# Kernel tuning notes

Hardware: AMD Instinct MI355X
Metric: run time of the kernel (lower is better)

The kernel has to match this reference:

```python
import jax, jax.numpy as jnp
import numpy as np

B = 4096
NUM_IMAGES = 10
D = 512
MARGIN = 1.0
EPS = 1e-6  # torch F.pairwise_distance adds eps to the difference elementwise


def _make_triplets():
    # per TripletLoss.generate_subsamples
    i = np.arange(B)
    j = np.arange(1, NUM_IMAGES)
    anchor = np.repeat(i, NUM_IMAGES - 1)                      # [T]
    positive = np.repeat(i * NUM_IMAGES, NUM_IMAGES - 1)       # [T]
    negative = (i[:, None] * NUM_IMAGES + j[None, :]).reshape(-1)  # [T]
    return anchor.astype(np.int64), positive.astype(np.int64), negative.astype(np.int64)


def setup_inputs() -> dict:
    key = jax.random.key(0)
    k1, k2 = jax.random.split(key)
    a, p, n = _make_triplets()
    return {
        "text_embeddings": jax.random.normal(k1, (B, D), dtype=jnp.float32),
        "image_embeddings": jax.random.normal(k2, (B * NUM_IMAGES, D), dtype=jnp.float32),
        "anchor_idx": jnp.asarray(a),
        "positive_idx": jnp.asarray(p),
        "negative_idx": jnpp if False else jnp.asarray(n),
    }


def _pairwise_dist(x, y):
    # torch pairwise_distance: ||x - y + eps||_2
    d = x - y + EPS
    return jnp.sqrt(jnp.sum(d * d, axis=-1))


def reference(text_embeddings, image_embeddings, anchor_idx, positive_idx, negative_idx):
    a = text_embeddings[anchor_idx]       # [T, D]
    p = image_embeddings[positive_idx]    # [T, D]
    n = image_embeddings[negative_idx]    # [T, D]
    d_ap = _pairwise_dist(a, p)           # [T]
    d_an = _pairwise_dist(a, n)           # [T]
    per_triplet = jnp.maximum(d_ap - d_an + MARGIN, 0.0)
    return jnp.mean(per_triplet)
```

## Files before the change

kernel.cpp:

```cpp
#include <hip/hip_runtime.h>


#define BATCH 4096
#define NIMG 10
#define DIM 512
#define NTRIP (BATCH * (NIMG - 1))

static constexpr float kMargin = 1.0f;
static constexpr float kEps = 1e-6f;

__global__ __launch_bounds__(256) void triplet_partial_kernel(
    const float* __restrict__ text,
    const float* __restrict__ img,
    float* __restrict__ partial)
{
    const int gtid = blockIdx.x * blockDim.x + threadIdx.x;
    const int wave = gtid >> 6;
    const int lane = threadIdx.x & 63;

    const float* arow = text + (size_t)wave * DIM + lane * 8;
    const float4 a0 = *(const float4*)(arow);
    const float4 a1 = *(const float4*)(arow + 4);

    const float* ibase = img + (size_t)wave * NIMG * DIM + lane * 8;

    float ssq[NIMG];
#pragma unroll
    for (int j = 0; j < NIMG; ++j) {
        const float* r = ibase + j * DIM;
        const float4 r0 = *(const float4*)(r);
        const float4 r1 = *(const float4*)(r + 4);
        float d0 = a0.x - r0.x + kEps;
        float d1 = a0.y - r0.y + kEps;
        float d2 = a0.z - r0.z + kEps;
        float d3 = a0.w - r0.w + kEps;
        float d4 = a1.x - r1.x + kEps;
        float d5 = a1.y - r1.y + kEps;
        float d6 = a1.z - r1.z + kEps;
        float d7 = a1.w - r1.w + kEps;
        float s = d0 * d0;
        s = fmaf(d1, d1, s);
        s = fmaf(d2, d2, s);
        s = fmaf(d3, d3, s);
        s = fmaf(d4, d4, s);
        s = fmaf(d5, d5, s);
        s = fmaf(d6, d6, s);
        s = fmaf(d7, d7, s);
        ssq[j] = s;
    }

#pragma unroll
    for (int j = 0; j < NIMG; ++j) {
        float v = ssq[j];
#pragma unroll
        for (int off = 32; off > 0; off >>= 1)
            v += __shfl_xor(v, off, 64);
        ssq[j] = v;
    }

    const float d_ap = sqrtf(ssq[0]);
    float loss = 0.0f;
#pragma unroll
    for (int j = 1; j < NIMG; ++j) {
        const float d_an = sqrtf(ssq[j]);
        loss += fmaxf(d_ap - d_an + kMargin, 0.0f);
    }

    if (lane == 0) partial[wave] = loss;
}

__global__ __launch_bounds__(1024) void triplet_reduce_kernel(
    const float* __restrict__ partial, float* __restrict__ out)
{
    __shared__ float wsum[16];
    const float4 v = *(const float4*)(partial + threadIdx.x * 4);
    float s = (v.x + v.y) + (v.z + v.w);
#pragma unroll
    for (int off = 32; off > 0; off >>= 1)
        s += __shfl_xor(s, off, 64);
    const int wid = threadIdx.x >> 6;
    const int lane = threadIdx.x & 63;
    if (lane == 0) wsum[wid] = s;
    __syncthreads();
    if (threadIdx.x < 16) {
        float t = wsum[threadIdx.x];
#pragma unroll
        for (int off = 8; off > 0; off >>= 1)
            t += __shfl_xor(t, off, 64);
        if (threadIdx.x == 0) out[0] = t * (1.0f / (float)NTRIP);
    }
}

extern "C" void kernel_launch(void* const* d_in, const int* in_sizes, int n_in,
                              void* d_out, int out_size, void* d_ws, size_t ws_size,
                              hipStream_t stream) {
    const float* text = (const float*)d_in[0];
    const float* img  = (const float*)d_in[1];
    float* out = (float*)d_out;
    float* partial = (float*)d_ws;

    const int threads = 256;
    const int blocks = BATCH / 4;
    triplet_partial_kernel<<<blocks, threads, 0, stream>>>(text, img, partial);
    triplet_reduce_kernel<<<1, 1024, 0, stream>>>(partial, out);
}
```

Measured before the change: 22.38 us.

## Fuse partial and final reduction into one cooperative kernel with grid sync

```diff
diff --git a/kernel.cpp b/kernel.cpp
--- a/kernel.cpp
+++ b/kernel.cpp
@@ -1,28 +1,30 @@
 #include <hip/hip_runtime.h>
+#include <hip/hip_cooperative_groups.h>
+
+namespace cg = cooperative_groups;
 
 
 #define BATCH 4096
 #define NIMG 10
 #define DIM 512
 #define NTRIP (BATCH * (NIMG - 1))
+#define NBLK 256
+#define THREADS 256
+#define WAVES_PER_BLK (THREADS / 64)
+#define ANCH_PER_WAVE (BATCH / (NBLK * WAVES_PER_BLK))
 
 static constexpr float kMargin = 1.0f;
 static constexpr float kEps = 1e-6f;
 
-__global__ __launch_bounds__(256) void triplet_partial_kernel(
-    const float* __restrict__ text,
-    const float* __restrict__ img,
-    float* __restrict__ partial)
+__device__ __forceinline__ float anchor_loss(
+    const float* __restrict__ text, const float* __restrict__ img,
+    int anchor, int lane)
 {
-    const int gtid = blockIdx.x * blockDim.x + threadIdx.x;
-    const int wave = gtid >> 6;
-    const int lane = threadIdx.x & 63;
-
-    const float* arow = text + (size_t)wave * DIM + lane * 8;
+    const float* arow = text + (size_t)anchor * DIM + lane * 8;
     const float4 a0 = *(const float4*)(arow);
     const float4 a1 = *(const float4*)(arow + 4);
 
-    const float* ibase = img + (size_t)wave * NIMG * DIM + lane * 8;
+    const float* ibase = img + (size_t)anchor * NIMG * DIM + lane * 8;
 
     float ssq[NIMG];
 #pragma unroll
@@ -65,7 +67,59 @@
         const float d_an = sqrtf(ssq[j]);
         loss += fmaxf(d_ap - d_an + kMargin, 0.0f);
     }
+    return loss;
+}
 
+__global__ __launch_bounds__(THREADS) void triplet_coop_kernel(
+    const float* __restrict__ text,
+    const float* __restrict__ img,
+    float* __restrict__ partial,
+    float* __restrict__ out)
+{
+    __shared__ float lsum[WAVES_PER_BLK];
+    __shared__ float wsum[WAVES_PER_BLK];
+
+    const int lane = threadIdx.x & 63;
+    const int wid  = threadIdx.x >> 6;
+    const int gwave = blockIdx.x * WAVES_PER_BLK + wid;
+
+    float wloss = 0.0f;
+#pragma unroll
+    for (int k = 0; k < ANCH_PER_WAVE; ++k)
+        wloss += anchor_loss(text, img, gwave * ANCH_PER_WAVE + k, lane);
+
+    if (lane == 0) lsum[wid] = wloss;
+    __syncthreads();
+    if (threadIdx.x == 0) {
+        const float bs = lsum[0] + lsum[1] + lsum[2] + lsum[3];
+        __hip_atomic_store(&partial[blockIdx.x], bs,
+                           __ATOMIC_RELAXED, __HIP_MEMORY_SCOPE_AGENT);
+    }
+
+    cg::this_grid().sync();
+
+    if (blockIdx.x == 0) {
+        float s = __hip_atomic_load(&partial[threadIdx.x],
+                                    __ATOMIC_RELAXED, __HIP_MEMORY_SCOPE_AGENT);
+#pragma unroll
+        for (int off = 32; off > 0; off >>= 1)
+            s += __shfl_xor(s, off, 64);
+        if (lane == 0) wsum[wid] = s;
+        __syncthreads();
+        if (threadIdx.x == 0)
+            out[0] = (wsum[0] + wsum[1] + wsum[2] + wsum[3]) * (1.0f / (float)NTRIP);
+    }
+}
+
+
+__global__ __launch_bounds__(256) void triplet_partial_kernel(
+    const float* __restrict__ text, const float* __restrict__ img,
+    float* __restrict__ partial)
+{
+    const int gtid = blockIdx.x * blockDim.x + threadIdx.x;
+    const int wave = gtid >> 6;
+    const int lane = threadIdx.x & 63;
+    const float loss = anchor_loss(text, img, wave, lane);
     if (lane == 0) partial[wave] = loss;
 }
 
@@ -99,8 +153,12 @@
     float* out = (float*)d_out;
     float* partial = (float*)d_ws;
 
-    const int threads = 256;
-    const int blocks = BATCH / 4;
-    triplet_partial_kernel<<<blocks, threads, 0, stream>>>(text, img, partial);
-    triplet_reduce_kernel<<<1, 1024, 0, stream>>>(partial, out);
+    void* args[] = {(void*)&text, (void*)&img, (void*)&partial, (void*)&out};
+    hipError_t err = hipLaunchCooperativeKernel(
+        (const void*)triplet_coop_kernel, dim3(NBLK), dim3(THREADS),
+        args, 0, stream);
+    if (err != hipSuccess) {
+        triplet_partial_kernel<<<BATCH / 4, 256, 0, stream>>>(text, img, partial);
+        triplet_reduce_kernel<<<1, 1024, 0, stream>>>(partial, out);
+    }
 }
```

Result: slower. 66.27 us (+196.1%).

## Split each anchor across two waves and reduce per block in LDS

Applied to the files above, without the earlier changes.

```diff
diff --git a/kernel.cpp b/kernel.cpp
--- a/kernel.cpp
+++ b/kernel.cpp
@@ -5,47 +5,44 @@
 #define NIMG 10
 #define DIM 512
 #define NTRIP (BATCH * (NIMG - 1))
+#define THREADS 1024
+#define ANCH_PER_BLK 8
+#define NBLK (BATCH / ANCH_PER_BLK)
 
 static constexpr float kMargin = 1.0f;
 static constexpr float kEps = 1e-6f;
 
-__global__ __launch_bounds__(256) void triplet_partial_kernel(
+__global__ __launch_bounds__(THREADS) void triplet_main_kernel(
     const float* __restrict__ text,
     const float* __restrict__ img,
     float* __restrict__ partial)
 {
-    const int gtid = blockIdx.x * blockDim.x + threadIdx.x;
-    const int wave = gtid >> 6;
+    __shared__ float halfsum[16 * NIMG];
+    __shared__ float fullsum[ANCH_PER_BLK * NIMG];
+    __shared__ float lossLds[ANCH_PER_BLK];
+
     const int lane = threadIdx.x & 63;
+    const int wid  = threadIdx.x >> 6;
+    const int aloc = wid >> 1;
+    const int half = wid & 1;
+    const int anchor = blockIdx.x * ANCH_PER_BLK + aloc;
+    const int off = half * 256 + lane * 4;
 
-    const float* arow = text + (size_t)wave * DIM + lane * 8;
-    const float4 a0 = *(const float4*)(arow);
-    const float4 a1 = *(const float4*)(arow + 4);
-
-    const float* ibase = img + (size_t)wave * NIMG * DIM + lane * 8;
+    const float4 a = *(const float4*)(text + (size_t)anchor * DIM + off);
+    const float* ibase = img + (size_t)anchor * NIMG * DIM + off;
 
     float ssq[NIMG];
 #pragma unroll
     for (int j = 0; j < NIMG; ++j) {
-        const float* r = ibase + j * DIM;
-        const float4 r0 = *(const float4*)(r);
-        const float4 r1 = *(const float4*)(r + 4);
-        float d0 = a0.x - r0.x + kEps;
-        float d1 = a0.y - r0.y + kEps;
-        float d2 = a0.z - r0.z + kEps;
-        float d3 = a0.w - r0.w + kEps;
-        float d4 = a1.x - r1.x + kEps;
-        float d5 = a1.y - r1.y + kEps;
-        float d6 = a1.z - r1.z + kEps;
-        float d7 = a1.w - r1.w + kEps;
+        const float4 r = *(const float4*)(ibase + j * DIM);
+        const float d0 = a.x - r.x + kEps;
+        const float d1 = a.y - r.y + kEps;
+        const float d2 = a.z - r.z + kEps;
+        const float d3 = a.w - r.w + kEps;
         float s = d0 * d0;
         s = fmaf(d1, d1, s);
         s = fmaf(d2, d2, s);
         s = fmaf(d3, d3, s);
-        s = fmaf(d4, d4, s);
-        s = fmaf(d5, d5, s);
-        s = fmaf(d6, d6, s);
-        s = fmaf(d7, d7, s);
         ssq[j] = s;
     }
 
@@ -53,41 +50,64 @@
     for (int j = 0; j < NIMG; ++j) {
         float v = ssq[j];
 #pragma unroll
-        for (int off = 32; off > 0; off >>= 1)
-            v += __shfl_xor(v, off, 64);
+        for (int o = 32; o > 0; o >>= 1)
+            v += __shfl_xor(v, o, 64);
         ssq[j] = v;
     }
 
-    const float d_ap = sqrtf(ssq[0]);
-    float loss = 0.0f;
+    if (lane == 0) {
 #pragma unroll
-    for (int j = 1; j < NIMG; ++j) {
-        const float d_an = sqrtf(ssq[j]);
-        loss += fmaxf(d_ap - d_an + kMargin, 0.0f);
+        for (int j = 0; j < NIMG; ++j)
+            halfsum[wid * NIMG + j] = ssq[j];
     }
+    __syncthreads();
 
-    if (lane == 0) partial[wave] = loss;
+    if (threadIdx.x < ANCH_PER_BLK * NIMG) {
+        const int ai = threadIdx.x / NIMG;
+        const int j  = threadIdx.x % NIMG;
+        fullsum[ai * NIMG + j] =
+            halfsum[(2 * ai) * NIMG + j] + halfsum[(2 * ai + 1) * NIMG + j];
+    }
+    __syncthreads();
+
+    if (threadIdx.x < ANCH_PER_BLK) {
+        const int ai = threadIdx.x;
+        const float d_ap = sqrtf(fullsum[ai * NIMG + 0]);
+        float loss = 0.0f;
+#pragma unroll
+        for (int j = 1; j < NIMG; ++j) {
+            const float d_an = sqrtf(fullsum[ai * NIMG + j]);
+            loss += fmaxf(d_ap - d_an + kMargin, 0.0f);
+        }
+        lossLds[ai] = loss;
+    }
+    __syncthreads();
+
+    if (threadIdx.x == 0) {
+        float bs = 0.0f;
+#pragma unroll
+        for (int ai = 0; ai < ANCH_PER_BLK; ++ai) bs += lossLds[ai];
+        partial[blockIdx.x] = bs;
+    }
 }
 
-__global__ __launch_bounds__(1024) void triplet_reduce_kernel(
+__global__ __launch_bounds__(512) void triplet_reduce_kernel(
     const float* __restrict__ partial, float* __restrict__ out)
 {
-    __shared__ float wsum[16];
-    const float4 v = *(const float4*)(partial + threadIdx.x * 4);
-    float s = (v.x + v.y) + (v.z + v.w);
+    __shared__ float wsum[8];
+    float s = partial[threadIdx.x];
 #pragma unroll
-    for (int off = 32; off > 0; off >>= 1)
-        s += __shfl_xor(s, off, 64);
+    for (int o = 32; o > 0; o >>= 1)
+        s += __shfl_xor(s, o, 64);
     const int wid = threadIdx.x >> 6;
     const int lane = threadIdx.x & 63;
     if (lane == 0) wsum[wid] = s;
     __syncthreads();
-    if (threadIdx.x < 16) {
-        float t = wsum[threadIdx.x];
+    if (threadIdx.x == 0) {
+        float t = 0.0f;
 #pragma unroll
-        for (int off = 8; off > 0; off >>= 1)
-            t += __shfl_xor(t, off, 64);
-        if (threadIdx.x == 0) out[0] = t * (1.0f / (float)NTRIP);
+        for (int w = 0; w < 8; ++w) t += wsum[w];
+        out[0] = t * (1.0f / (float)NTRIP);
     }
 }
 
@@ -99,8 +119,6 @@
     float* out = (float*)d_out;
     float* partial = (float*)d_ws;
 
-    const int threads = 256;
-    const int blocks = BATCH / 4;
-    triplet_partial_kernel<<<blocks, threads, 0, stream>>>(text, img, partial);
-    triplet_reduce_kernel<<<1, 1024, 0, stream>>>(partial, out);
+    triplet_main_kernel<<<NBLK, THREADS, 0, stream>>>(text, img, partial);
+    triplet_reduce_kernel<<<1, 512, 0, stream>>>(partial, out);
 }
```

New measurement: 21.55 us. 3.7% less time.
